# Performance work log

Measured on AMD Instinct MI355X. Metric: run time of the kernel, lower is better.

Reference implementation:

```python
import jax, jax.numpy as jnp
import numpy as np
import math

TOP_K = 2          # args.k
CAP_FACTOR = 1.0   # args.f
MIN_CAPACITY = 1


def setup_inputs() -> dict:
    key = jax.random.key(0)
    k1, k2 = jax.random.split(key)
    inp = jax.random.normal(k1, (8192, 2048), dtype=jnp.float32)        # tokens x M
    wg_weight = jax.random.normal(k2, (64, 2048), dtype=jnp.float32) * 0.02  # E x M (torch Linear layout)
    return {"inp": inp, "wg_weight": wg_weight}


def _top1gating(logits):
    S, E = logits.shape
    # _capacity: ceil(S/E * f), clamped to min_capacity, then scaled by top_k
    capacity = TOP_K * max(int(math.ceil(S / E * CAP_FACTOR)), MIN_CAPACITY)

    gates = jax.nn.softmax(logits, axis=1)                 # [S, E]
    indices1_s = jnp.argmax(gates, axis=1)                 # [S]
    mask1 = jax.nn.one_hot(indices1_s, E, dtype=jnp.int32) # [S, E]

    # keep only the first `capacity` tokens per expert (torch.topk over dim 0 of the 0/1 mask;
    _, top_idx = jax.lax.top_k(mask1.T, capacity)          # [E, C] token indices
    keep = jnp.zeros_like(mask1).at[top_idx.T, jnp.arange(E)[None, :]].set(1)  # scatter dim0
    mask1 = mask1 * keep                                   # drop overflow tokens

    # position of each kept token within its expert's capacity buffer
    locations1 = jnp.cumsum(mask1, axis=0) - 1             # [S, E]
    locations1_s = jnp.sum(locations1 * mask1, axis=1)     # [S] int

    gates = gates * mask1.astype(gates.dtype)              # zero gates of dropped tokens
    locations1_sc = jax.nn.one_hot(locations1_s, capacity, dtype=gates.dtype)  # [S, C]

    combine_weights = jnp.einsum('se,sc->sec', gates, locations1_sc)  # [S, E, C]
    dispatch_mask = combine_weights.astype(bool)
    return combine_weights, dispatch_mask


def reference(inp, wg_weight):
    x = inp.reshape(-1, inp.shape[-1])          # [S, M]
    logits = x @ wg_weight.T                    # [S, E]
    return _top1gating(logits)
```

## Files before the change

kernel.cpp:

```cpp
#include <hip/hip_runtime.h>
#include <hip/hip_bf16.h>

#define S_TOK 8192
#define NEXP 64
#define NK 2048
#define CAP 256

__global__ __launch_bounds__(256) void fill_zero(float4* __restrict__ out, long long n4) {
    long long i = (long long)blockIdx.x * blockDim.x + threadIdx.x;
    long long stride = (long long)gridDim.x * blockDim.x;
    float4 z = make_float4(0.f, 0.f, 0.f, 0.f);
    for (; i < n4; i += stride) out[i] = z;
}

__global__ __launch_bounds__(256) void gemm_logits(const float* __restrict__ x,
                                                   const float* __restrict__ w,
                                                   float* __restrict__ logits) {
    __shared__ float xs[64][65];
    __shared__ float ws[64][65];
    const int t = threadIdx.x;
    const int block_t0 = blockIdx.x * 64;
    const int te = (t & 15) * 4;
    const int tt = (t >> 4) * 4;

    float acc[4][4];
#pragma unroll
    for (int i = 0; i < 4; ++i)
#pragma unroll
        for (int j = 0; j < 4; ++j) acc[i][j] = 0.f;

    for (int k0 = 0; k0 < NK; k0 += 64) {
#pragma unroll
        for (int i = 0; i < 4; ++i) {
            int lin  = t + i * 256;
            int row  = lin >> 4;
            int col4 = (lin & 15) * 4;
            float4 v = *reinterpret_cast<const float4*>(&x[(long long)(block_t0 + row) * NK + k0 + col4]);
            xs[row][col4 + 0] = v.x; xs[row][col4 + 1] = v.y;
            xs[row][col4 + 2] = v.z; xs[row][col4 + 3] = v.w;
            float4 u = *reinterpret_cast<const float4*>(&w[(long long)row * NK + k0 + col4]);
            ws[row][col4 + 0] = u.x; ws[row][col4 + 1] = u.y;
            ws[row][col4 + 2] = u.z; ws[row][col4 + 3] = u.w;
        }
        __syncthreads();
#pragma unroll
        for (int k = 0; k < 64; ++k) {
            float xv[4], wv[4];
#pragma unroll
            for (int i = 0; i < 4; ++i) xv[i] = xs[tt + i][k];
#pragma unroll
            for (int j = 0; j < 4; ++j) wv[j] = ws[te + j][k];
#pragma unroll
            for (int i = 0; i < 4; ++i)
#pragma unroll
                for (int j = 0; j < 4; ++j) acc[i][j] = fmaf(xv[i], wv[j], acc[i][j]);
        }
        __syncthreads();
    }
#pragma unroll
    for (int i = 0; i < 4; ++i)
#pragma unroll
        for (int j = 0; j < 4; ++j)
            logits[(long long)(block_t0 + tt + i) * NEXP + te + j] = acc[i][j];
}

__global__ __launch_bounds__(256) void gate_argmax(const float* __restrict__ logits,
                                                   int* __restrict__ eidx,
                                                   float* __restrict__ gate) {
    const int lane = threadIdx.x & 63;
    const int tok = blockIdx.x * 4 + (threadIdx.x >> 6);
    float l = logits[(long long)tok * NEXP + lane];

    float m = l; int mi = lane;
#pragma unroll
    for (int off = 32; off; off >>= 1) {
        float om  = __shfl_xor(m, off);
        int   omi = __shfl_xor(mi, off);
        if (om > m || (om == m && omi < mi)) { m = om; mi = omi; }
    }
    float e = expf(l - m);
    float s = e;
#pragma unroll
    for (int off = 32; off; off >>= 1) s += __shfl_xor(s, off);

    if (lane == 0) {
        eidx[tok] = mi;
        gate[tok] = 1.0f / s;
    }
}

__global__ __launch_bounds__(64) void cap_scatter(const int* __restrict__ eidx,
                                                  const float* __restrict__ gate,
                                                  float* __restrict__ out,
                                                  long long dispOff) {
    const int e = blockIdx.x;
    const int lane = threadIdx.x;
    int count = 0;
    for (int s0 = 0; s0 < S_TOK; s0 += 64) {
        int s = s0 + lane;
        bool match = (eidx[s] == e);
        unsigned long long b = __ballot(match);
        int rank = count + __popcll(b & ((1ull << lane) - 1ull));
        if (match && rank < CAP) {
            long long o = (long long)s * (NEXP * CAP) + (long long)e * CAP + rank;
            out[o] = gate[s];
            out[dispOff + o] = 1.0f;
        }
        count += __popcll(b);
    }
}

extern "C" void kernel_launch(void* const* d_in, const int* in_sizes, int n_in,
                              void* d_out, int out_size, void* d_ws, size_t ws_size,
                              hipStream_t stream) {
    const float* x = (const float*)d_in[0];
    const float* w = (const float*)d_in[1];
    float* out = (float*)d_out;

    float* logits = (float*)d_ws;
    int*   eidx   = (int*)((char*)d_ws + (size_t)S_TOK * NEXP * 4);
    float* gate   = (float*)((char*)eidx + (size_t)S_TOK * 4);

    const long long total = (long long)out_size;
    const long long dispOff = total / 2;

    fill_zero<<<4096, 256, 0, stream>>>((float4*)out, total / 4);

    gemm_logits<<<S_TOK / 64, 256, 0, stream>>>(x, w, logits);

    gate_argmax<<<S_TOK / 4, 256, 0, stream>>>(logits, eidx, gate);

    cap_scatter<<<NEXP, 64, 0, stream>>>(eidx, gate, out, dispOff);
}
```

Before: 1.303 ms.

## Split-K logits GEMM, parallel rank, and fused dense output write

Replaces the zero-fill plus sparse scatter with a kernel that writes every output element exactly once, folding the zeros and the gate values into one pass. The logits GEMM becomes a split-K (two halves) kernel that streams weights from global/cache per wave, and the partials are summed in the argmax kernel. Per-expert ranking now runs with 1024 threads using a block-level prefix sum instead of a serial 64-thread loop. This aims to remove the separate zero pass and the serial scatter. The cost is extra partial-logit traffic and uncached weight loads in the GEMM inner loop.

Result: no change. 1.318 ms (+1.2%).

```diff
diff --git a/kernel.cpp b/kernel.cpp
--- a/kernel.cpp
+++ b/kernel.cpp
@@ -6,70 +6,62 @@
 #define NK 2048
 #define CAP 256
 
-__global__ __launch_bounds__(256) void fill_zero(float4* __restrict__ out, long long n4) {
-    long long i = (long long)blockIdx.x * blockDim.x + threadIdx.x;
-    long long stride = (long long)gridDim.x * blockDim.x;
-    float4 z = make_float4(0.f, 0.f, 0.f, 0.f);
-    for (; i < n4; i += stride) out[i] = z;
-}
-
 __global__ __launch_bounds__(256) void gemm_logits(const float* __restrict__ x,
                                                    const float* __restrict__ w,
-                                                   float* __restrict__ logits) {
-    __shared__ float xs[64][65];
-    __shared__ float ws[64][65];
+                                                   float* __restrict__ part) {
+    __shared__ float xs[64][132];
     const int t = threadIdx.x;
-    const int block_t0 = blockIdx.x * 64;
-    const int te = (t & 15) * 4;
-    const int tt = (t >> 4) * 4;
+    const int lane = t & 63;
+    const int wv = __builtin_amdgcn_readfirstlane(t >> 6);
+    const int e_base = wv * 16;
+    const int tg = blockIdx.x & 127;
+    const int kz = blockIdx.x >> 7;
+    const int s0 = tg * 64;
+    const long long koff = (long long)kz * 1024;
 
-    float acc[4][4];
+    float acc[16];
 #pragma unroll
-    for (int i = 0; i < 4; ++i)
+    for (int j = 0; j < 16; ++j) acc[j] = 0.f;
+
+    for (int k0 = 0; k0 < 1024; k0 += 128) {
 #pragma unroll
-        for (int j = 0; j < 4; ++j) acc[i][j] = 0.f;
-
-    for (int k0 = 0; k0 < NK; k0 += 64) {
-#pragma unroll
-        for (int i = 0; i < 4; ++i) {
-            int lin  = t + i * 256;
-            int row  = lin >> 4;
-            int col4 = (lin & 15) * 4;
-            float4 v = *reinterpret_cast<const float4*>(&x[(long long)(block_t0 + row) * NK + k0 + col4]);
-            xs[row][col4 + 0] = v.x; xs[row][col4 + 1] = v.y;
-            xs[row][col4 + 2] = v.z; xs[row][col4 + 3] = v.w;
-            float4 u = *reinterpret_cast<const float4*>(&w[(long long)row * NK + k0 + col4]);
-            ws[row][col4 + 0] = u.x; ws[row][col4 + 1] = u.y;
-            ws[row][col4 + 2] = u.z; ws[row][col4 + 3] = u.w;
+        for (int i = 0; i < 8; ++i) {
+            int lin = t + i * 256;
+            int row = lin >> 5;
+            int c4  = lin & 31;
+            float4 v = *reinterpret_cast<const float4*>(
+                &x[(long long)(s0 + row) * NK + koff + k0 + c4 * 4]);
+            *reinterpret_cast<float4*>(&xs[row][c4 * 4]) = v;
         }
         __syncthreads();
+#pragma unroll 2
+        for (int kk = 0; kk < 128; kk += 4) {
+            float4 xv = *reinterpret_cast<const float4*>(&xs[lane][kk]);
 #pragma unroll
-        for (int k = 0; k < 64; ++k) {
-            float xv[4], wv[4];
-#pragma unroll
-            for (int i = 0; i < 4; ++i) xv[i] = xs[tt + i][k];
-#pragma unroll
-            for (int j = 0; j < 4; ++j) wv[j] = ws[te + j][k];
-#pragma unroll
-            for (int i = 0; i < 4; ++i)
-#pragma unroll
-                for (int j = 0; j < 4; ++j) acc[i][j] = fmaf(xv[i], wv[j], acc[i][j]);
+            for (int j = 0; j < 16; ++j) {
+                const float* wr = w + (long long)(e_base + j) * NK + koff + k0 + kk;
+                acc[j] = fmaf(xv.x, wr[0], acc[j]);
+                acc[j] = fmaf(xv.y, wr[1], acc[j]);
+                acc[j] = fmaf(xv.z, wr[2], acc[j]);
+                acc[j] = fmaf(xv.w, wr[3], acc[j]);
+            }
         }
         __syncthreads();
     }
-#pragma unroll
-    for (int i = 0; i < 4; ++i)
-#pragma unroll
-        for (int j = 0; j < 4; ++j)
-            logits[(long long)(block_t0 + tt + i) * NEXP + te + j] = acc[i][j];
+    float* dst = part + (long long)kz * (S_TOK * NEXP) + (long long)(s0 + lane) * NEXP + e_base;
+    *reinterpret_cast<float4*>(&dst[0])  = make_float4(acc[0], acc[1], acc[2], acc[3]);
+    *reinterpret_cast<float4*>(&dst[4])  = make_float4(acc[4], acc[5], acc[6], acc[7]);
+    *reinterpret_cast<float4*>(&dst[8])  = make_float4(acc[8], acc[9], acc[10], acc[11]);
+    *reinterpret_cast<float4*>(&dst[12]) = make_float4(acc[12], acc[13], acc[14], acc[15]);
 }
 
-__global__ __launch_bounds__(256) void gate_argmax(const float* __restrict__ logits,
+__global__ __launch_bounds__(256) void gate_argmax(const float* __restrict__ part,
                                                    int* __restrict__ eidx,
                                                    float* __restrict__ gate) {
     const int lane = threadIdx.x & 63;
     const int tok = blockIdx.x * 4 + (threadIdx.x >> 6);
-    float l = logits[(long long)tok * NEXP + lane];
+    long long o = (long long)tok * NEXP + lane;
+    float l = part[o] + part[(long long)(S_TOK * NEXP) + o];
 
     float m = l; int mi = lane;
 #pragma unroll
@@ -89,25 +81,69 @@
     }
 }
 
-__global__ __launch_bounds__(64) void cap_scatter(const int* __restrict__ eidx,
-                                                  const float* __restrict__ gate,
-                                                  float* __restrict__ out,
-                                                  long long dispOff) {
+__global__ __launch_bounds__(1024) void rank_tokens(const int* __restrict__ eidx,
+                                                    int* __restrict__ pack) {
+    __shared__ int cnts[16];
     const int e = blockIdx.x;
-    const int lane = threadIdx.x;
-    int count = 0;
-    for (int s0 = 0; s0 < S_TOK; s0 += 64) {
-        int s = s0 + lane;
-        bool match = (eidx[s] == e);
-        unsigned long long b = __ballot(match);
-        int rank = count + __popcll(b & ((1ull << lane) - 1ull));
-        if (match && rank < CAP) {
-            long long o = (long long)s * (NEXP * CAP) + (long long)e * CAP + rank;
-            out[o] = gate[s];
-            out[dispOff + o] = 1.0f;
+    const int t = threadIdx.x;
+    const int lane = t & 63;
+    const int v = __builtin_amdgcn_readfirstlane(t >> 6);
+    const int base = v * 512;
+
+    int cnt = 0;
+#pragma unroll
+    for (int i = 0; i < 8; ++i) {
+        int s = base + i * 64 + lane;
+        unsigned long long b = __ballot(eidx[s] == e);
+        cnt += __popcll(b);
+    }
+    if (lane == 0) cnts[v] = cnt;
+    __syncthreads();
+    if (t == 0) {
+        int run = 0;
+#pragma unroll
+        for (int j = 0; j < 16; ++j) { int c = cnts[j]; cnts[j] = run; run += c; }
+    }
+    __syncthreads();
+    int run = cnts[v];
+#pragma unroll
+    for (int i = 0; i < 8; ++i) {
+        int s = base + i * 64 + lane;
+        bool m = (eidx[s] == e);
+        unsigned long long b = __ballot(m);
+        if (m) {
+            int r = run + __popcll(b & ((1ull << lane) - 1ull));
+            pack[s] = (r < CAP) ? ((r << 6) | e) : -1;
         }
-        count += __popcll(b);
+        run += __popcll(b);
     }
+}
+
+__global__ __launch_bounds__(256) void write_out(const int* __restrict__ pack,
+                                                 const float* __restrict__ gate,
+                                                 float* __restrict__ out) {
+    const int t = threadIdx.x;
+    const int lane = t & 63;
+    const int wv = __builtin_amdgcn_readfirstlane(t >> 6);
+    const int row = blockIdx.x * 4 + wv;
+    const int s = row >> 6;
+    const int e = row & 63;
+
+    const int info = pack[s];
+    const float g = gate[s];
+
+    float4 c4 = make_float4(0.f, 0.f, 0.f, 0.f);
+    float4 d4 = make_float4(0.f, 0.f, 0.f, 0.f);
+    if (info >= 0 && (info & 63) == e) {
+        int r = info >> 6;
+        if ((r >> 2) == lane) {
+            ((float*)&c4)[r & 3] = g;
+            ((float*)&d4)[r & 3] = 1.0f;
+        }
+    }
+    long long o = (long long)row * CAP + lane * 4;
+    *reinterpret_cast<float4*>(&out[o]) = c4;
+    *reinterpret_cast<float4*>(&out[(long long)S_TOK * NEXP * CAP + o]) = d4;
 }
 
 extern "C" void kernel_launch(void* const* d_in, const int* in_sizes, int n_in,
@@ -117,18 +153,13 @@
     const float* w = (const float*)d_in[1];
     float* out = (float*)d_out;
 
-    float* logits = (float*)d_ws;
-    int*   eidx   = (int*)((char*)d_ws + (size_t)S_TOK * NEXP * 4);
-    float* gate   = (float*)((char*)eidx + (size_t)S_TOK * 4);
+    float* part = (float*)d_ws;
+    int*   eidx = (int*)((char*)d_ws + (size_t)2 * S_TOK * NEXP * 4);
+    float* gate = (float*)((char*)eidx + (size_t)S_TOK * 4);
+    int*   pack = (int*)((char*)gate + (size_t)S_TOK * 4);
 
-    const long long total = (long long)out_size;
-    const long long dispOff = total / 2;
-
-    fill_zero<<<4096, 256, 0, stream>>>((float4*)out, total / 4);
-
-    gemm_logits<<<S_TOK / 64, 256, 0, stream>>>(x, w, logits);
-
-    gate_argmax<<<S_TOK / 4, 256, 0, stream>>>(logits, eidx, gate);
-
-    cap_scatter<<<NEXP, 64, 0, stream>>>(eidx, gate, out, dispOff);
+    gemm_logits<<<256, 256, 0, stream>>>(x, w, part);
+    gate_argmax<<<S_TOK / 4, 256, 0, stream>>>(part, eidx, gate);
+    rank_tokens<<<NEXP, 1024, 0, stream>>>(eidx, pack);
+    write_out<<<(S_TOK * NEXP) / 4, 256, 0, stream>>>(pack, gate, out);
 }
```
